# Kernel optimization log

Hardware: AMD Instinct MI355X
Metric: run time of the kernel (lower is better)

## Reference

```python
import jax, jax.numpy as jnp
import numpy as np

N_NODES = 100000
NEG_SLOPE = 0.01  # torch F.leaky_relu default


def sage_gcn_layer(feat, src, dst, W, b):
    # DGL SAGEConv, aggregator_type='gcn':
    #   h_i = fc_neigh((sum_{j->i} x_j + x_i) / (in_deg_i + 1))
    neigh_sum = jax.ops.segment_sum(feat[src], dst, num_segments=N_NODES)
    deg = jax.ops.segment_sum(jnp.ones((src.shape[0],), feat.dtype), dst,
                              num_segments=N_NODES)
    h = (neigh_sum + feat) / (deg + 1.0)[:, None]
    return h @ W + b


def setup_inputs() -> dict:
    key = jax.random.key(0)
    k_feat, k_e, k_w1, k_w2 = jax.random.split(key, 4)
    d_in, d_hid, d_out = 128, 128, 128
    E = 1600000
    feat = jax.random.normal(k_feat, (N_NODES, d_in), dtype=jnp.float32)
    edge_index = jax.random.randint(k_e, (2, E), 0, N_NODES, dtype=jnp.int64)
    W1 = jax.random.normal(k_w1, (d_in, d_hid), dtype=jnp.float32) / np.sqrt(d_in)
    b1 = jnp.zeros((d_hid,), jnp.float32)
    W2 = jax.random.normal(k_w2, (d_hid, d_out), dtype=jnp.float32) / np.sqrt(d_hid)
    b2 = jnp.zeros((d_out,), jnp.float32)
    return {"feat": feat, "edge_index": edge_index,
            "W1": W1, "b1": b1, "W2": W2, "b2": b2}


def reference(feat, edge_index, W1, b1, W2, b2):
    src, dst = edge_index[0], edge_index[1]
    h = sage_gcn_layer(feat, src, dst, W1, b1)
    h = jax.nn.leaky_relu(h, NEG_SLOPE)
    # dropout = 0 -> identity
    h = sage_gcn_layer(h, src, dst, W2, b2)
    return jax.nn.leaky_relu(h, NEG_SLOPE)
```

## Files before the change

### kernel.cpp

```cpp
#include <hip/hip_runtime.h>

#define NEG_SLOPE 0.01f
#define BSHIFT 8
#define BMASK 255
#define BMAX 512
#define CAPB 5120

typedef __attribute__((ext_vector_type(8))) short bf16x8;
typedef __attribute__((ext_vector_type(4))) float f32x4;
typedef __attribute__((ext_vector_type(2))) float f32x2;
typedef __attribute__((ext_vector_type(4))) unsigned u32x4;

static __device__ inline unsigned short f2b(float f) {
    unsigned u = __builtin_bit_cast(unsigned, f);
    return (unsigned short)((u + 0x7FFF + ((u >> 16) & 1)) >> 16);
}
static __device__ inline float b2f_lo(unsigned u) {
    return __builtin_bit_cast(float, u << 16);
}
static __device__ inline float b2f_hi(unsigned u) {
    return __builtin_bit_cast(float, u & 0xFFFF0000u);
}

__global__ __launch_bounds__(256) void front_kernel(const float* __restrict__ feat,
                                                    unsigned short* __restrict__ featb,
                                                    long long nfeat,
                                                    const float* __restrict__ W1,
                                                    const float* __restrict__ W2,
                                                    unsigned short* __restrict__ Wt1,
                                                    unsigned short* __restrict__ Wt2,
                                                    int* __restrict__ bcursor,
                                                    int B, int nf4) {
    const int bx = blockIdx.x;
    const int t = threadIdx.x;
    if (bx < nf4) {
        long long i = ((long long)bx * 256 + t) * 4;
        if (i < nfeat) {
            float4 v = *(const float4*)(feat + i);
            ushort4 o;
            o.x = f2b(v.x); o.y = f2b(v.y); o.z = f2b(v.z); o.w = f2b(v.w);
            *(ushort4*)(featb + i) = o;
        }
        return;
    }
    const int bx2 = bx - nf4;
    if (bx2 < 2) {
        int z = bx2 * 256 + t;
        if (z < BMAX) bcursor[z] = 0;
    }
    int i = bx2 * 256 + t;
    int n = i & 127, k = i >> 7;
    Wt1[n * 128 + k] = f2b(W1[k * 128 + n]);
    Wt2[n * 128 + k] = f2b(W2[k * 128 + n]);
}

__global__ __launch_bounds__(256) void bscatter_kernel(const int* __restrict__ src,
                                                       const int* __restrict__ dst,
                                                       int* __restrict__ bcursor,
                                                       unsigned* __restrict__ pairs,
                                                       int E, int B) {
    __shared__ int h[BMAX];
    __shared__ int base[BMAX];
    const int t = threadIdx.x;
    for (int i = t; i < B; i += 256) h[i] = 0;
    __syncthreads();
    const int chunk = (E + gridDim.x - 1) / gridDim.x;
    const int e0 = blockIdx.x * chunk;
    const int e1 = min(e0 + chunk, E);
    for (int e = e0 + t; e < e1; e += 256)
        atomicAdd(&h[dst[e] >> BSHIFT], 1);
    __syncthreads();
    for (int i = t; i < B; i += 256) {
        int c = h[i];
        base[i] = c ? atomicAdd(&bcursor[i], c) : 0;
    }
    __syncthreads();
    for (int i = t; i < B; i += 256) h[i] = base[i];
    __syncthreads();
    for (int e = e0 + t; e < e1; e += 256) {
        int d = dst[e];
        int b = d >> BSHIFT;
        int pos = atomicAdd(&h[b], 1);
        if (pos < CAPB)
            pairs[(size_t)b * CAPB + pos] = (unsigned)src[e] | ((unsigned)(d & BMASK) << 24);
    }
}

__global__ __launch_bounds__(256) void bfinal_kernel(const unsigned* __restrict__ pairs,
                                                     const int* __restrict__ bcursor,
                                                     int* __restrict__ offsets,
                                                     int* __restrict__ degs,
                                                     int* __restrict__ csr, int N) {
    __shared__ int h[256];
    __shared__ int cur[256];
    const int b = blockIdx.x;
    const int t = threadIdx.x;
    const int cnt = min(bcursor[b], CAPB);
    const unsigned* __restrict__ pb = pairs + (size_t)b * CAPB;
    h[t] = 0;
    __syncthreads();
    for (int e = t; e < cnt; e += 256)
        atomicAdd(&h[pb[e] >> 24], 1);
    __syncthreads();
    int v = h[t];
    for (int d = 1; d < 256; d <<= 1) {
        int u = (t >= d) ? h[t - d] : 0;
        __syncthreads();
        h[t] += u;
        __syncthreads();
    }
    const int prefix = h[t] - v;
    const int node = (b << BSHIFT) + t;
    if (node < N) {
        offsets[node] = b * CAPB + prefix;
        degs[node] = v;
    }
    cur[t] = prefix;
    __syncthreads();
    int* __restrict__ cb = csr + (size_t)b * CAPB;
    for (int e = t; e < cnt; e += 256) {
        unsigned pr = pb[e];
        int pos = atomicAdd(&cur[pr >> 24], 1);
        cb[pos] = (int)(pr & 0xFFFFFFu);
    }
}

static __device__ inline f32x2 up2(unsigned u) {
    return (f32x2){ b2f_lo(u), b2f_hi(u) };
}

#define GATHER(dst, off) \
    asm volatile("global_load_dwordx4 %0, %1, %2" : "=v"(dst) : "v"(off), "s"(xc))
#define ACC4(u) do { A0 += up2((u).x); A1 += up2((u).y); \
                     A2 += up2((u).z); A3 += up2((u).w); } while (0)
#define ACCM(u, mk) do { \
    A0 += up2((u).x & (mk)); A1 += up2((u).y & (mk)); \
    A2 += up2((u).z & (mk)); A3 += up2((u).w & (mk)); } while (0)

static __device__ __forceinline__ unsigned rowsel(int g, unsigned poff,
                                                  int i0, int i1, int i2, int i3) {
    int s01 = (g & 1) ? i1 : i0;
    int s23 = (g & 1) ? i3 : i2;
    int s = (g & 2) ? s23 : s01;
    return ((unsigned)s << 8) | poff;
}

__global__ __launch_bounds__(256) void aggregate_kernel(const unsigned short* __restrict__ xb,
                                                        const int* __restrict__ offsets,
                                                        const int* __restrict__ degs,
                                                        const int* __restrict__ csr,
                                                        unsigned short* __restrict__ Hb,
                                                        int N) {
    const int node = (blockIdx.x * blockDim.x + threadIdx.x) >> 6;
    if (node >= N) return;
    const int lane = threadIdx.x & 63;
    const int g = lane >> 4;
    const unsigned poff = (unsigned)((lane & 15) << 4);
    const char* __restrict__ xc = (const char*)xb;

    const int nu = __builtin_amdgcn_readfirstlane(node);
    const int start = __builtin_amdgcn_readfirstlane(offsets[nu]);
    const int deg   = __builtin_amdgcn_readfirstlane(degs[nu]);
    const int rounds = deg >> 2;
    const int tailn  = deg & 3;

    u32x4 vs = (u32x4){0, 0, 0, 0};
    if (g == 0) GATHER(vs, ((unsigned)nu << 8) | poff);

    f32x2 A0 = {0.f, 0.f}, A1 = {0.f, 0.f}, A2 = {0.f, 0.f}, A3 = {0.f, 0.f};

    int r = 0;
    while (r + 4 <= rounds) {
        const int p = start + (r << 2);
        int i0  = csr[p +  0], i1  = csr[p +  1], i2  = csr[p +  2], i3  = csr[p +  3];
        int i4  = csr[p +  4], i5  = csr[p +  5], i6  = csr[p +  6], i7  = csr[p +  7];
        int i8  = csr[p +  8], i9  = csr[p +  9], i10 = csr[p + 10], i11 = csr[p + 11];
        int i12 = csr[p + 12], i13 = csr[p + 13], i14 = csr[p + 14], i15 = csr[p + 15];
        unsigned a0 = rowsel(g, poff, i0,  i1,  i2,  i3);
        unsigned a1 = rowsel(g, poff, i4,  i5,  i6,  i7);
        unsigned a2 = rowsel(g, poff, i8,  i9,  i10, i11);
        unsigned a3 = rowsel(g, poff, i12, i13, i14, i15);
        __builtin_amdgcn_sched_barrier(0);
        u32x4 v0, v1, v2, v3;
        GATHER(v0, a0); GATHER(v1, a1); GATHER(v2, a2); GATHER(v3, a3);
        asm volatile("s_waitcnt vmcnt(0)" ::: "memory");
        __builtin_amdgcn_sched_barrier(0);
        ACC4(v0); ACC4(v1); ACC4(v2); ACC4(v3);
        r += 4;
    }

    const int rr = rounds - r;
    const int p = start + (r << 2);
    u32x4 v0, v1, v2, vt;
    if (rr >= 1) {
        int i0 = csr[p + 0], i1 = csr[p + 1], i2 = csr[p + 2], i3 = csr[p + 3];
        GATHER(v0, rowsel(g, poff, i0, i1, i2, i3));
    }
    if (rr >= 2) {
        int i0 = csr[p + 4], i1 = csr[p + 5], i2 = csr[p + 6], i3 = csr[p + 7];
        GATHER(v1, rowsel(g, poff, i0, i1, i2, i3));
    }
    if (rr >= 3) {
        int i0 = csr[p + 8], i1 = csr[p + 9], i2 = csr[p + 10], i3 = csr[p + 11];
        GATHER(v2, rowsel(g, poff, i0, i1, i2, i3));
    }
    const unsigned mt = (g < tailn) ? ~0u : 0u;
    if (tailn) {
        const int q = start + (rounds << 2);
        int t0 = csr[q];
        int t1 = (tailn > 1) ? csr[q + 1] : t0;
        int t2 = (tailn > 2) ? csr[q + 2] : t0;
        GATHER(vt, rowsel(g, poff, t0, t1, t2, t0));
    }
    asm volatile("s_waitcnt vmcnt(0)" ::: "memory");
    __builtin_amdgcn_sched_barrier(0);
    if (rr >= 1) ACC4(v0);
    if (rr >= 2) ACC4(v1);
    if (rr >= 3) ACC4(v2);
    if (tailn) ACCM(vt, mt);

    float a[8];
    a[0] = A0.x; a[1] = A0.y; a[2] = A1.x; a[3] = A1.y;
    a[4] = A2.x; a[5] = A2.y; a[6] = A3.x; a[7] = A3.y;
#pragma unroll
    for (int i = 0; i < 8; ++i) {
        a[i] += __shfl_xor(a[i], 16);
        a[i] += __shfl_xor(a[i], 32);
    }
    a[0] += b2f_lo(vs.x); a[1] += b2f_hi(vs.x);
    a[2] += b2f_lo(vs.y); a[3] += b2f_hi(vs.y);
    a[4] += b2f_lo(vs.z); a[5] += b2f_hi(vs.z);
    a[6] += b2f_lo(vs.w); a[7] += b2f_hi(vs.w);

    const float inv = 1.0f / (float)(deg + 1);
    if (g == 0) {
        uint4 o;
        o.x = (unsigned)f2b(a[0] * inv) | ((unsigned)f2b(a[1] * inv) << 16);
        o.y = (unsigned)f2b(a[2] * inv) | ((unsigned)f2b(a[3] * inv) << 16);
        o.z = (unsigned)f2b(a[4] * inv) | ((unsigned)f2b(a[5] * inv) << 16);
        o.w = (unsigned)f2b(a[6] * inv) | ((unsigned)f2b(a[7] * inv) << 16);
        *(uint4*)((char*)Hb + (((unsigned)node << 8) | poff)) = o;
    }
}

template <bool OUT_BF16>
__global__ __launch_bounds__(256) void gemm_mfma(const unsigned short* __restrict__ Hb,
                                                 const unsigned short* __restrict__ Wt,
                                                 const float* __restrict__ b,
                                                 void* __restrict__ outv, int N) {
    __shared__ unsigned short Wa[128 * 128];
    const int tid = threadIdx.x;
    const int row0 = blockIdx.x * 128;

#pragma unroll
    for (int it = 0; it < 8; ++it) {
        int idx = it * 256 + tid;
        int r = idx >> 4, c = idx & 15;
        uint4 v = *(const uint4*)(Wt + r * 128 + c * 8);
        *(uint4*)(Wa + r * 128 + ((c ^ (r & 15)) << 3)) = v;
    }
    __syncthreads();

    const int w = tid >> 6;
    const int lane = tid & 63;
    const int m = lane & 15;
    const int q = lane >> 4;

    const int r0 = row0 + w * 32 + m;
    const size_t ar0 = (size_t)min(r0, N - 1) * 128;
    const size_t ar1 = (size_t)min(r0 + 16, N - 1) * 128;

    f32x4 acc[2][8];
#pragma unroll
    for (int rt = 0; rt < 2; ++rt)
#pragma unroll
        for (int ct = 0; ct < 8; ++ct) acc[rt][ct] = (f32x4){0.f, 0.f, 0.f, 0.f};

#pragma unroll
    for (int kk = 0; kk < 4; ++kk) {
        const int chunk = kk * 4 + q;
        bf16x8 af0 = *(const bf16x8*)(Hb + ar0 + chunk * 8);
        bf16x8 af1 = *(const bf16x8*)(Hb + ar1 + chunk * 8);
#pragma unroll
        for (int ct = 0; ct < 8; ++ct) {
            int n = ct * 16 + m;
            bf16x8 bfr = *(const bf16x8*)(Wa + n * 128 + ((chunk ^ (n & 15)) << 3));
            acc[0][ct] = __builtin_amdgcn_mfma_f32_16x16x32_bf16(af0, bfr, acc[0][ct], 0, 0, 0);
            acc[1][ct] = __builtin_amdgcn_mfma_f32_16x16x32_bf16(af1, bfr, acc[1][ct], 0, 0, 0);
        }
    }

#pragma unroll
    for (int ct = 0; ct < 8; ++ct) {
        const float bias = b[ct * 16 + m];
        const int gcol = ct * 16 + m;
#pragma unroll
        for (int rt = 0; rt < 2; ++rt) {
#pragma unroll
            for (int reg = 0; reg < 4; ++reg) {
                int grow = row0 + w * 32 + rt * 16 + q * 4 + reg;
                if (grow < N) {
                    float v = acc[rt][ct][reg] + bias;
                    v = v > 0.f ? v : v * NEG_SLOPE;
                    if (OUT_BF16)
                        ((unsigned short*)outv)[(long long)grow * 128 + gcol] = f2b(v);
                    else
                        ((float*)outv)[(long long)grow * 128 + gcol] = v;
                }
            }
        }
    }
}

extern "C" void kernel_launch(void* const* d_in, const int* in_sizes, int n_in,
                              void* d_out, int out_size, void* d_ws, size_t ws_size,
                              hipStream_t stream) {
    const float* feat = (const float*)d_in[0];
    const int*   edges = (const int*)d_in[1];
    const float* W1 = (const float*)d_in[2];
    const float* b1 = (const float*)d_in[3];
    const float* W2 = (const float*)d_in[4];
    const float* b2 = (const float*)d_in[5];
    float* out = (float*)d_out;

    const int N = in_sizes[0] / 128;
    const int E = in_sizes[1] / 2;
    const int* src = edges;
    const int* dst = edges + E;
    const int B = (N + (1 << BSHIFT) - 1) >> BSHIFT;

    unsigned short* featb = (unsigned short*)d_ws;
    unsigned short* Hb    = featb + (size_t)N * 128;
    unsigned*       pairs = (unsigned*)Hb;
    unsigned short* Wt1   = Hb + (size_t)N * 128;
    unsigned short* Wt2   = Wt1 + 128 * 128;
    int* offsets = (int*)(Wt2 + 128 * 128);
    int* degs    = offsets + ((N + 8) & ~7);
    int* bcursor = degs + ((N + 8) & ~7);
    int* csr     = bcursor + 512;

    const long long nfeat = (long long)N * 128;
    const int nf4 = (int)((nfeat / 4 + 255) / 256);

    front_kernel<<<nf4 + 64, 256, 0, stream>>>(feat, featb, nfeat, W1, W2,
                                               Wt1, Wt2, bcursor, B, nf4);
    bscatter_kernel<<<256, 256, 0, stream>>>(src, dst, bcursor, pairs, E, B);
    bfinal_kernel<<<B, 256, 0, stream>>>(pairs, bcursor, offsets, degs, csr, N);

    const int aggGrid = (N + 3) / 4;
    const int gemmGrid = (N + 127) / 128;

    aggregate_kernel<<<aggGrid, 256, 0, stream>>>(featb, offsets, degs, csr, Hb, N);
    gemm_mfma<true><<<gemmGrid, 256, 0, stream>>>(Hb, Wt1, b1, (void*)featb, N);

    aggregate_kernel<<<aggGrid, 256, 0, stream>>>(featb, offsets, degs, csr, Hb, N);
    gemm_mfma<false><<<gemmGrid, 256, 0, stream>>>(Hb, Wt2, b2, (void*)out, N);
}
```

Baseline: 313.3 us.

## Fuse bucket scatter and per-bucket sort into one cooperative kernel

Merges the bucket-scatter and bucket-finalize CSR build kernels into a single cooperative launch with a grid-wide sync between the phases. Each block then stages its bucket into shared memory, sorts it by destination locally and writes the result back in place, so the separate pairs buffer and one kernel launch go away. In exchange it needs a cooperative launch of B (~391) blocks with about 42KB of shared memory each, which limits occupancy and adds grid-sync cost. The scatter phase also now runs on B blocks instead of 256.

```diff
diff --git a/kernel.cpp b/kernel.cpp
--- a/kernel.cpp
+++ b/kernel.cpp
@@ -1,4 +1,7 @@
 #include <hip/hip_runtime.h>
+#include <hip/hip_cooperative_groups.h>
+
+namespace cg = cooperative_groups;
 
 #define NEG_SLOPE 0.01f
 #define BSHIFT 8
@@ -54,18 +57,23 @@
     Wt2[n * 128 + k] = f2b(W2[k * 128 + n]);
 }
 
-__global__ __launch_bounds__(256) void bscatter_kernel(const int* __restrict__ src,
-                                                       const int* __restrict__ dst,
-                                                       int* __restrict__ bcursor,
-                                                       unsigned* __restrict__ pairs,
-                                                       int E, int B) {
-    __shared__ int h[BMAX];
-    __shared__ int base[BMAX];
+__global__ __launch_bounds__(256) void csr_build(const int* __restrict__ src,
+                                                 const int* __restrict__ dst,
+                                                 int* __restrict__ bcursor,
+                                                 unsigned* __restrict__ csrU,
+                                                 int* __restrict__ offsets,
+                                                 int* __restrict__ degs,
+                                                 int E, int B, int N) {
+    __shared__ int smem[2 * CAPB + 512];
     const int t = threadIdx.x;
+    const int b = blockIdx.x;
+
+    int* h = smem;
+    int* base = smem + BMAX;
     for (int i = t; i < B; i += 256) h[i] = 0;
     __syncthreads();
-    const int chunk = (E + gridDim.x - 1) / gridDim.x;
-    const int e0 = blockIdx.x * chunk;
+    const int chunk = (E + (int)gridDim.x - 1) / (int)gridDim.x;
+    const int e0 = b * chunk;
     const int e1 = min(e0 + chunk, E);
     for (int e = e0 + t; e < e1; e += 256)
         atomicAdd(&h[dst[e] >> BSHIFT], 1);
@@ -79,37 +87,34 @@
     __syncthreads();
     for (int e = e0 + t; e < e1; e += 256) {
         int d = dst[e];
-        int b = d >> BSHIFT;
-        int pos = atomicAdd(&h[b], 1);
+        int bb = d >> BSHIFT;
+        int pos = atomicAdd(&h[bb], 1);
         if (pos < CAPB)
-            pairs[(size_t)b * CAPB + pos] = (unsigned)src[e] | ((unsigned)(d & BMASK) << 24);
-    }
-}
-
-__global__ __launch_bounds__(256) void bfinal_kernel(const unsigned* __restrict__ pairs,
-                                                     const int* __restrict__ bcursor,
-                                                     int* __restrict__ offsets,
-                                                     int* __restrict__ degs,
-                                                     int* __restrict__ csr, int N) {
-    __shared__ int h[256];
-    __shared__ int cur[256];
-    const int b = blockIdx.x;
-    const int t = threadIdx.x;
+            csrU[(size_t)bb * CAPB + pos] = (unsigned)src[e] | ((unsigned)(d & BMASK) << 24);
+    }
+
+    cg::this_grid().sync();
+
+    unsigned* stage  = (unsigned*)smem;
+    unsigned* sorted = (unsigned*)smem + CAPB;
+    int* h2  = smem + 2 * CAPB;
+    int* cur = h2 + 256;
     const int cnt = min(bcursor[b], CAPB);
-    const unsigned* __restrict__ pb = pairs + (size_t)b * CAPB;
-    h[t] = 0;
+    unsigned* __restrict__ cb = csrU + (size_t)b * CAPB;
+    for (int e = t; e < cnt; e += 256) stage[e] = cb[e];
+    h2[t] = 0;
     __syncthreads();
     for (int e = t; e < cnt; e += 256)
-        atomicAdd(&h[pb[e] >> 24], 1);
-    __syncthreads();
-    int v = h[t];
+        atomicAdd(&h2[stage[e] >> 24], 1);
+    __syncthreads();
+    int v = h2[t];
     for (int d = 1; d < 256; d <<= 1) {
-        int u = (t >= d) ? h[t - d] : 0;
+        int u = (t >= d) ? h2[t - d] : 0;
         __syncthreads();
-        h[t] += u;
+        h2[t] += u;
         __syncthreads();
     }
-    const int prefix = h[t] - v;
+    const int prefix = h2[t] - v;
     const int node = (b << BSHIFT) + t;
     if (node < N) {
         offsets[node] = b * CAPB + prefix;
@@ -117,12 +122,13 @@
     }
     cur[t] = prefix;
     __syncthreads();
-    int* __restrict__ cb = csr + (size_t)b * CAPB;
     for (int e = t; e < cnt; e += 256) {
-        unsigned pr = pb[e];
+        unsigned pr = stage[e];
         int pos = atomicAdd(&cur[pr >> 24], 1);
-        cb[pos] = (int)(pr & 0xFFFFFFu);
-    }
+        sorted[pos] = pr & 0xFFFFFFu;
+    }
+    __syncthreads();
+    for (int e = t; e < cnt; e += 256) cb[e] = sorted[e];
 }
 
 static __device__ inline f32x2 up2(unsigned u) {
@@ -331,7 +337,6 @@
 
     unsigned short* featb = (unsigned short*)d_ws;
     unsigned short* Hb    = featb + (size_t)N * 128;
-    unsigned*       pairs = (unsigned*)Hb;
     unsigned short* Wt1   = Hb + (size_t)N * 128;
     unsigned short* Wt2   = Wt1 + 128 * 128;
     int* offsets = (int*)(Wt2 + 128 * 128);
@@ -344,8 +349,21 @@
 
     front_kernel<<<nf4 + 64, 256, 0, stream>>>(feat, featb, nfeat, W1, W2,
                                                Wt1, Wt2, bcursor, B, nf4);
-    bscatter_kernel<<<256, 256, 0, stream>>>(src, dst, bcursor, pairs, E, B);
-    bfinal_kernel<<<B, 256, 0, stream>>>(pairs, bcursor, offsets, degs, csr, N);
+
+    {
+        const int* srca = src;
+        const int* dsta = dst;
+        int* bca = bcursor;
+        unsigned* csrUa = (unsigned*)csr;
+        int* offa = offsets;
+        int* dega = degs;
+        int Ea = E, Ba = B, Na = N;
+        void* kargs[] = {(void*)&srca, (void*)&dsta, (void*)&bca, (void*)&csrUa,
+                         (void*)&offa, (void*)&dega, (void*)&Ea, (void*)&Ba,
+                         (void*)&Na};
+        hipLaunchCooperativeKernel((const void*)csr_build, dim3(B), dim3(256),
+                                   kargs, 0, stream);
+    }
 
     const int aggGrid = (N + 3) / 4;
     const int gemmGrid = (N + 127) / 128;
```

New measurement: 385.3 us. +23.0%, slower.

## Apply weight matrix before aggregation and fuse bias/activation into aggregate

Applied to the files above, without the earlier changes.

Uses associativity to compute X·W first with an fp32-input MFMA GEMM, then aggregates the transformed features and applies mean normalisation, bias and leaky ReLU inside the aggregation kernel. This drops the separate fp32-to-bf16 feature conversion pass and the bias/activation epilogue in the GEMM. The bucket scatter kernel now caches destination indices in shared memory and uses a fixed per-block edge chunk, which increases the grid size. Rounding order changes because bf16 rounding now happens after the matmul rather than before.

```diff
diff --git a/kernel.cpp b/kernel.cpp
--- a/kernel.cpp
+++ b/kernel.cpp
@@ -5,6 +5,7 @@
 #define BMASK 255
 #define BMAX 512
 #define CAPB 5120
+#define SCCH 6144
 
 typedef __attribute__((ext_vector_type(8))) short bf16x8;
 typedef __attribute__((ext_vector_type(4))) float f32x4;
@@ -22,33 +23,13 @@
     return __builtin_bit_cast(float, u & 0xFFFF0000u);
 }
 
-__global__ __launch_bounds__(256) void front_kernel(const float* __restrict__ feat,
-                                                    unsigned short* __restrict__ featb,
-                                                    long long nfeat,
-                                                    const float* __restrict__ W1,
+__global__ __launch_bounds__(256) void front_kernel(const float* __restrict__ W1,
                                                     const float* __restrict__ W2,
                                                     unsigned short* __restrict__ Wt1,
                                                     unsigned short* __restrict__ Wt2,
-                                                    int* __restrict__ bcursor,
-                                                    int B, int nf4) {
-    const int bx = blockIdx.x;
-    const int t = threadIdx.x;
-    if (bx < nf4) {
-        long long i = ((long long)bx * 256 + t) * 4;
-        if (i < nfeat) {
-            float4 v = *(const float4*)(feat + i);
-            ushort4 o;
-            o.x = f2b(v.x); o.y = f2b(v.y); o.z = f2b(v.z); o.w = f2b(v.w);
-            *(ushort4*)(featb + i) = o;
-        }
-        return;
-    }
-    const int bx2 = bx - nf4;
-    if (bx2 < 2) {
-        int z = bx2 * 256 + t;
-        if (z < BMAX) bcursor[z] = 0;
-    }
-    int i = bx2 * 256 + t;
+                                                    int* __restrict__ bcursor) {
+    int i = blockIdx.x * 256 + threadIdx.x;
+    if (i < BMAX) bcursor[i] = 0;
     int n = i & 127, k = i >> 7;
     Wt1[n * 128 + k] = f2b(W1[k * 128 + n]);
     Wt2[n * 128 + k] = f2b(W2[k * 128 + n]);
@@ -61,14 +42,17 @@
                                                        int E, int B) {
     __shared__ int h[BMAX];
     __shared__ int base[BMAX];
+    __shared__ int dl[SCCH];
     const int t = threadIdx.x;
     for (int i = t; i < B; i += 256) h[i] = 0;
     __syncthreads();
-    const int chunk = (E + gridDim.x - 1) / gridDim.x;
-    const int e0 = blockIdx.x * chunk;
-    const int e1 = min(e0 + chunk, E);
-    for (int e = e0 + t; e < e1; e += 256)
-        atomicAdd(&h[dst[e] >> BSHIFT], 1);
+    const int e0 = blockIdx.x * SCCH;
+    const int e1 = min(e0 + SCCH, E);
+    for (int e = e0 + t; e < e1; e += 256) {
+        int d = dst[e];
+        dl[e - e0] = d;
+        atomicAdd(&h[d >> BSHIFT], 1);
+    }
     __syncthreads();
     for (int i = t; i < B; i += 256) {
         int c = h[i];
@@ -78,11 +62,11 @@
     for (int i = t; i < B; i += 256) h[i] = base[i];
     __syncthreads();
     for (int e = e0 + t; e < e1; e += 256) {
-        int d = dst[e];
-        int b = d >> BSHIFT;
-        int pos = atomicAdd(&h[b], 1);
+        int d = dl[e - e0];
+        int bb = d >> BSHIFT;
+        int pos = atomicAdd(&h[bb], 1);
         if (pos < CAPB)
-            pairs[(size_t)b * CAPB + pos] = (unsigned)src[e] | ((unsigned)(d & BMASK) << 24);
+            pairs[(size_t)bb * CAPB + pos] = (unsigned)src[e] | ((unsigned)(d & BMASK) << 24);
     }
 }
 
@@ -125,6 +109,86 @@
     }
 }
 
+template <bool IN_F32>
+__global__ __launch_bounds__(256) void gemm_xw(const void* __restrict__ inA,
+                                               const unsigned short* __restrict__ Wt,
+                                               unsigned short* __restrict__ outy,
+                                               int N) {
+    __shared__ unsigned short Wa[128 * 128];
+    const int tid = threadIdx.x;
+    const int row0 = blockIdx.x * 128;
+
+#pragma unroll
+    for (int it = 0; it < 8; ++it) {
+        int idx = it * 256 + tid;
+        int r = idx >> 4, c = idx & 15;
+        uint4 v = *(const uint4*)(Wt + r * 128 + c * 8);
+        *(uint4*)(Wa + r * 128 + ((c ^ (r & 15)) << 3)) = v;
+    }
+    __syncthreads();
+
+    const int w = tid >> 6;
+    const int lane = tid & 63;
+    const int m = lane & 15;
+    const int q = lane >> 4;
+
+    const int r0 = row0 + w * 32 + m;
+    const size_t ar0 = (size_t)min(r0, N - 1) * 128;
+    const size_t ar1 = (size_t)min(r0 + 16, N - 1) * 128;
+
+    f32x4 acc[2][8];
+#pragma unroll
+    for (int rt = 0; rt < 2; ++rt)
+#pragma unroll
+        for (int ct = 0; ct < 8; ++ct) acc[rt][ct] = (f32x4){0.f, 0.f, 0.f, 0.f};
+
+#pragma unroll
+    for (int kk = 0; kk < 4; ++kk) {
+        const int chunk = kk * 4 + q;
+        bf16x8 af0, af1;
+        if (IN_F32) {
+            const float* Af = (const float*)inA;
+            float4 u0 = *(const float4*)(Af + ar0 + chunk * 8);
+            float4 u1 = *(const float4*)(Af + ar0 + chunk * 8 + 4);
+            float4 u2 = *(const float4*)(Af + ar1 + chunk * 8);
+            float4 u3 = *(const float4*)(Af + ar1 + chunk * 8 + 4);
+            af0[0] = (short)f2b(u0.x); af0[1] = (short)f2b(u0.y);
+            af0[2] = (short)f2b(u0.z); af0[3] = (short)f2b(u0.w);
+            af0[4] = (short)f2b(u1.x); af0[5] = (short)f2b(u1.y);
+            af0[6] = (short)f2b(u1.z); af0[7] = (short)f2b(u1.w);
+            af1[0] = (short)f2b(u2.x); af1[1] = (short)f2b(u2.y);
+            af1[2] = (short)f2b(u2.z); af1[3] = (short)f2b(u2.w);
+            af1[4] = (short)f2b(u3.x); af1[5] = (short)f2b(u3.y);
+            af1[6] = (short)f2b(u3.z); af1[7] = (short)f2b(u3.w);
+        } else {
+            const unsigned short* Ab = (const unsigned short*)inA;
+            af0 = *(const bf16x8*)(Ab + ar0 + chunk * 8);
+            af1 = *(const bf16x8*)(Ab + ar1 + chunk * 8);
+        }
+#pragma unroll
+        for (int ct = 0; ct < 8; ++ct) {
+            int n = ct * 16 + m;
+            bf16x8 bfr = *(const bf16x8*)(Wa + n * 128 + ((chunk ^ (n & 15)) << 3));
+            acc[0][ct] = __builtin_amdgcn_mfma_f32_16x16x32_bf16(af0, bfr, acc[0][ct], 0, 0, 0);
+            acc[1][ct] = __builtin_amdgcn_mfma_f32_16x16x32_bf16(af1, bfr, acc[1][ct], 0, 0, 0);
+        }
+    }
+
+#pragma unroll
+    for (int ct = 0; ct < 8; ++ct) {
+        const int gcol = ct * 16 + m;
+#pragma unroll
+        for (int rt = 0; rt < 2; ++rt) {
+#pragma unroll
+            for (int reg = 0; reg < 4; ++reg) {
+                int grow = row0 + w * 32 + rt * 16 + q * 4 + reg;
+                if (grow < N)
+                    outy[(long long)grow * 128 + gcol] = f2b(acc[rt][ct][reg]);
+            }
+        }
+    }
+}
+
 static __device__ inline f32x2 up2(unsigned u) {
     return (f32x2){ b2f_lo(u), b2f_hi(u) };
 }
@@ -145,12 +209,13 @@
     return ((unsigned)s << 8) | poff;
 }
 
-__global__ __launch_bounds__(256) void aggregate_kernel(const unsigned short* __restrict__ xb,
-                                                        const int* __restrict__ offsets,
-                                                        const int* __restrict__ degs,
-                                                        const int* __restrict__ csr,
-                                                        unsigned short* __restrict__ Hb,
-                                                        int N) {
+template <bool OUT_F32>
+__global__ __launch_bounds__(256) void agg_apply(const unsigned short* __restrict__ xb,
+                                                 const int* __restrict__ offsets,
+                                                 const int* __restrict__ degs,
+                                                 const int* __restrict__ csr,
+                                                 const float* __restrict__ bias,
+                                                 void* __restrict__ outv, int N) {
     const int node = (blockIdx.x * blockDim.x + threadIdx.x) >> 6;
     if (node >= N) return;
     const int lane = threadIdx.x & 63;
@@ -234,80 +299,27 @@
 
     const float inv = 1.0f / (float)(deg + 1);
     if (g == 0) {
-        uint4 o;
-        o.x = (unsigned)f2b(a[0] * inv) | ((unsigned)f2b(a[1] * inv) << 16);
-        o.y = (unsigned)f2b(a[2] * inv) | ((unsigned)f2b(a[3] * inv) << 16);
-        o.z = (unsigned)f2b(a[4] * inv) | ((unsigned)f2b(a[5] * inv) << 16);
-        o.w = (unsigned)f2b(a[6] * inv) | ((unsigned)f2b(a[7] * inv) << 16);
-        *(uint4*)((char*)Hb + (((unsigned)node << 8) | poff)) = o;
-    }
-}
-
-template <bool OUT_BF16>
-__global__ __launch_bounds__(256) void gemm_mfma(const unsigned short* __restrict__ Hb,
-                                                 const unsigned short* __restrict__ Wt,
-                                                 const float* __restrict__ b,
-                                                 void* __restrict__ outv, int N) {
-    __shared__ unsigned short Wa[128 * 128];
-    const int tid = threadIdx.x;
-    const int row0 = blockIdx.x * 128;
-
-#pragma unroll
-    for (int it = 0; it < 8; ++it) {
-        int idx = it * 256 + tid;
-        int r = idx >> 4, c = idx & 15;
-        uint4 v = *(const uint4*)(Wt + r * 128 + c * 8);
-        *(uint4*)(Wa + r * 128 + ((c ^ (r & 15)) << 3)) = v;
-    }
-    __syncthreads();
-
-    const int w = tid >> 6;
-    const int lane = tid & 63;
-    const int m = lane & 15;
-    const int q = lane >> 4;
-
-    const int r0 = row0 + w * 32 + m;
-    const size_t ar0 = (size_t)min(r0, N - 1) * 128;
-    const size_t ar1 = (size_t)min(r0 + 16, N - 1) * 128;
-
-    f32x4 acc[2][8];
-#pragma unroll
-    for (int rt = 0; rt < 2; ++rt)
-#pragma unroll
-        for (int ct = 0; ct < 8; ++ct) acc[rt][ct] = (f32x4){0.f, 0.f, 0.f, 0.f};
-
-#pragma unroll
-    for (int kk = 0; kk < 4; ++kk) {
-        const int chunk = kk * 4 + q;
-        bf16x8 af0 = *(const bf16x8*)(Hb + ar0 + chunk * 8);
-        bf16x8 af1 = *(const bf16x8*)(Hb + ar1 + chunk * 8);
-#pragma unroll
-        for (int ct = 0; ct < 8; ++ct) {
-            int n = ct * 16 + m;
-            bf16x8 bfr = *(const bf16x8*)(Wa + n * 128 + ((chunk ^ (n & 15)) << 3));
-            acc[0][ct] = __builtin_amdgcn_mfma_f32_16x16x32_bf16(af0, bfr, acc[0][ct], 0, 0, 0);
-            acc[1][ct] = __builtin_amdgcn_mfma_f32_16x16x32_bf16(af1, bfr, acc[1][ct], 0, 0, 0);
-        }
-    }
-
-#pragma unroll
-    for (int ct = 0; ct < 8; ++ct) {
-        const float bias = b[ct * 16 + m];
-        const int gcol = ct * 16 + m;
-#pragma unroll
-        for (int rt = 0; rt < 2; ++rt) {
-#pragma unroll
-            for (int reg = 0; reg < 4; ++reg) {
-                int grow = row0 + w * 32 + rt * 16 + q * 4 + reg;
-                if (grow < N) {
-                    float v = acc[rt][ct][reg] + bias;
-                    v = v > 0.f ? v : v * NEG_SLOPE;
-                    if (OUT_BF16)
-                        ((unsigned short*)outv)[(long long)grow * 128 + gcol] = f2b(v);
-                    else
-                        ((float*)outv)[(long long)grow * 128 + gcol] = v;
-                }
-            }
+        const int c0 = (lane & 15) << 3;
+        const float4 bb0 = *(const float4*)(bias + c0);
+        const float4 bb1 = *(const float4*)(bias + c0 + 4);
+        float rv[8];
+        rv[0] = a[0] * inv + bb0.x; rv[1] = a[1] * inv + bb0.y;
+        rv[2] = a[2] * inv + bb0.z; rv[3] = a[3] * inv + bb0.w;
+        rv[4] = a[4] * inv + bb1.x; rv[5] = a[5] * inv + bb1.y;
+        rv[6] = a[6] * inv + bb1.z; rv[7] = a[7] * inv + bb1.w;
+#pragma unroll
+        for (int k = 0; k < 8; ++k) rv[k] = rv[k] > 0.f ? rv[k] : rv[k] * NEG_SLOPE;
+        if (OUT_F32) {
+            float* op = (float*)outv + (size_t)node * 128 + c0;
+            *(float4*)op = make_float4(rv[0], rv[1], rv[2], rv[3]);
+            *(float4*)(op + 4) = make_float4(rv[4], rv[5], rv[6], rv[7]);
+        } else {
+            uint4 o;
+            o.x = (unsigned)f2b(rv[0]) | ((unsigned)f2b(rv[1]) << 16);
+            o.y = (unsigned)f2b(rv[2]) | ((unsigned)f2b(rv[3]) << 16);
+            o.z = (unsigned)f2b(rv[4]) | ((unsigned)f2b(rv[5]) << 16);
+            o.w = (unsigned)f2b(rv[6]) | ((unsigned)f2b(rv[7]) << 16);
+            *(uint4*)((char*)outv + (((unsigned)node << 8) | poff)) = o;
         }
     }
 }
@@ -329,30 +341,27 @@
     const int* dst = edges + E;
     const int B = (N + (1 << BSHIFT) - 1) >> BSHIFT;
 
-    unsigned short* featb = (unsigned short*)d_ws;
-    unsigned short* Hb    = featb + (size_t)N * 128;
-    unsigned*       pairs = (unsigned*)Hb;
-    unsigned short* Wt1   = Hb + (size_t)N * 128;
-    unsigned short* Wt2   = Wt1 + 128 * 128;
+    unsigned short* T1  = (unsigned short*)d_ws;
+    unsigned short* T2  = T1 + (size_t)N * 128;
+    unsigned*       pairs = (unsigned*)T2;
+    unsigned short* Wt1 = T2 + (size_t)N * 128;
+    unsigned short* Wt2 = Wt1 + 128 * 128;
     int* offsets = (int*)(Wt2 + 128 * 128);
     int* degs    = offsets + ((N + 8) & ~7);
     int* bcursor = degs + ((N + 8) & ~7);
     int* csr     = bcursor + 512;
 
-    const long long nfeat = (long long)N * 128;
-    const int nf4 = (int)((nfeat / 4 + 255) / 256);
-
-    front_kernel<<<nf4 + 64, 256, 0, stream>>>(feat, featb, nfeat, W1, W2,
-                                               Wt1, Wt2, bcursor, B, nf4);
-    bscatter_kernel<<<256, 256, 0, stream>>>(src, dst, bcursor, pairs, E, B);
+    const int gemmGrid = (N + 127) / 128;
+    const int aggGrid  = (N + 3) / 4;
+    const int scGrid   = (E + SCCH - 1) / SCCH;
+
+    front_kernel<<<64, 256, 0, stream>>>(W1, W2, Wt1, Wt2, bcursor);
+    gemm_xw<true><<<gemmGrid, 256, 0, stream>>>(feat, Wt1, T1, N);
+    bscatter_kernel<<<scGrid, 256, 0, stream>>>(src, dst, bcursor, pairs, E, B);
     bfinal_kernel<<<B, 256, 0, stream>>>(pairs, bcursor, offsets, degs, csr, N);
-
-    const int aggGrid = (N + 3) / 4;
-    const int gemmGrid = (N + 127) / 128;
-
-    aggregate_kernel<<<aggGrid, 256, 0, stream>>>(featb, offsets, degs, csr, Hb, N);
-    gemm_mfma<true><<<gemmGrid, 256, 0, stream>>>(Hb, Wt1, b1, (void*)featb, N);
-
-    aggregate_kernel<<<aggGrid, 256, 0, stream>>>(featb, offsets, degs, csr, Hb, N);
-    gemm_mfma<false><<<gemmGrid, 256, 0, stream>>>(Hb, Wt2, b2, (void*)out, N);
-}
+    agg_apply<false><<<aggGrid, 256, 0, stream>>>(T1, offsets, degs, csr, b1,
+                                                  (void*)T2, N);
+    gemm_xw<false><<<gemmGrid, 256, 0, stream>>>(T2, Wt2, T1, N);
+    agg_apply<true><<<aggGrid, 256, 0, stream>>>(T1, offsets, degs, csr, b2,
+                                                 (void*)out, N);
+}
```

Result: faster. 299.1 us (-4.5%).
